# Kernel tuning notes

Hardware: AMD Instinct MI355X
Metric: run time of the kernel (lower is better)

Reference implementation:

```python
import jax, jax.numpy as jnp
import numpy as np

N, E, ET = 50000, 400000, 50000
F, ED, H, L = 64, 32, 128, 2


def _forward(x, edge_attr, target_edge_attr, node_W, node_b, edge_W, edge_b,
             pre_W, pre_b, post_W, post_b, lin_W, lin_b, bn_g, bn_b,
             em1_W, em1_b, em2_W, em2_b, edge_index):
    n = x.shape[0]
    h = node_W.shape[1]
    src, dst = edge_index[0], edge_index[1]
    x = x @ node_W + node_b                      # [N,H]
    ea = edge_attr @ edge_W + edge_b             # [E,H]
    tea = target_edge_attr @ edge_W + edge_b     # [Et,H]

    ones = jnp.ones((src.shape[0],), jnp.float32)
    cnt = jax.ops.segment_sum(ones, dst, num_segments=n)        # in-degree per node
    avg_deg_log = jnp.mean(jnp.log(cnt + 1.0))                  # PyG avg_deg['log'] from deg histogram
    deg = jnp.clip(cnt, 1.0)[:, None]
    amp = jnp.log(deg + 1.0) / avg_deg_log                      # 'amplification' scaler
    att = avg_deg_log / jnp.log(deg + 1.0)                      # 'attenuation' scaler
    cnt_c = jnp.clip(cnt, 1.0)[:, None]
    has = (cnt > 0)[:, None]

    nlayers = pre_W.shape[0]
    for i in range(nlayers):
        # pre-MLP on message cat([x_i(dst), x_j(src), edge_attr]); split matmul avoids [E,3H] concat
        Wd, Ws, We = pre_W[i, :h], pre_W[i, h:2 * h], pre_W[i, 2 * h:]
        m = x[dst] @ Wd + x[src] @ Ws + ea @ We + pre_b[i]      # [E,H]
        s = jax.ops.segment_sum(m, dst, num_segments=n)
        mean = s / cnt_c
        mean2 = jax.ops.segment_sum(m * m, dst, num_segments=n) / cnt_c
        std = jnp.sqrt(jax.nn.relu(mean2 - mean * mean) + 1e-5)  # PyG StdAggregation
        mn = jnp.where(has, jax.ops.segment_min(m, dst, num_segments=n), 0.0)
        mx = jnp.where(has, jax.ops.segment_max(m, dst, num_segments=n), 0.0)
        agg = jnp.concatenate([mean, mn, mx, std], axis=-1)     # [N,4H] aggregator order
        scaled = jnp.concatenate([agg, agg * amp, agg * att], axis=-1)  # [N,12H] scaler order
        # post-MLP on cat([x, scaled]); split matmul
        out = x @ post_W[i, :h] + scaled @ post_W[i, h:] + post_b[i]
        out = out @ lin_W[i] + lin_b[i]
        # BatchNorm (training mode, biased var, eps=1e-5)
        mu = out.mean(axis=0)
        var = jnp.mean((out - mu) ** 2, axis=0)
        bn = bn_g[i] * (out - mu) / jnp.sqrt(var + 1e-5) + bn_b[i]
        x = (x + jax.nn.relu(bn)) / 2
        # edge update: ea + MLP(cat([x[src], x[dst], ea])) / 2
        W1s, W1d, W1e = em1_W[i, :h], em1_W[i, h:2 * h], em1_W[i, 2 * h:]
        hid = jax.nn.relu(x[src] @ W1s + x[dst] @ W1d + ea @ W1e + em1_b[i])
        ea = ea + (hid @ em2_W[i] + em2_b[i]) / 2
    return (x, ea, tea)


def setup_inputs() -> dict:
    key = jax.random.key(0)
    ks = jax.random.split(key, 24)

    def w(k, shape):
        fan_in = shape[-2]
        return (jax.random.normal(k, shape, jnp.float32) / np.sqrt(fan_in)).astype(jnp.float32)

    inp = {
        'x': jax.random.normal(ks[0], (N, F), jnp.float32),
        'edge_attr': jax.random.normal(ks[1], (E, ED), jnp.float32),
        'target_edge_attr': jax.random.normal(ks[2], (ET, ED), jnp.float32),
        'node_W': w(ks[3], (F, H)), 'node_b': jnp.zeros((H,), jnp.float32),
        'edge_W': w(ks[4], (ED, H)), 'edge_b': jnp.zeros((H,), jnp.float32),
        'pre_W': w(ks[5], (L, 3 * H, H)), 'pre_b': jnp.zeros((L, H), jnp.float32),
        'post_W': w(ks[6], (L, 13 * H, H)), 'post_b': jnp.zeros((L, H), jnp.float32),
        'lin_W': w(ks[7], (L, H, H)), 'lin_b': jnp.zeros((L, H), jnp.float32),
        'bn_g': jnp.ones((L, H), jnp.float32), 'bn_b': jnp.zeros((L, H), jnp.float32),
        'em1_W': w(ks[8], (L, 3 * H, H)), 'em1_b': jnp.zeros((L, H), jnp.float32),
        'em2_W': w(ks[9], (L, H, H)), 'em2_b': jnp.zeros((L, H), jnp.float32),
        'edge_index': jax.random.randint(ks[10], (2, E), 0, N, dtype=jnp.int32),
    }
    return inp


def reference(x, edge_attr, target_edge_attr, node_W, node_b, edge_W, edge_b,
              pre_W, pre_b, post_W, post_b, lin_W, lin_b, bn_g, bn_b,
              em1_W, em1_b, em2_W, em2_b, edge_index):
    return _forward(x, edge_attr, target_edge_attr, node_W, node_b, edge_W, edge_b,
                    pre_W, pre_b, post_W, post_b, lin_W, lin_b, bn_g, bn_b,
                    em1_W, em1_b, em2_W, em2_b, edge_index)
```

## Files before the change

kernel.cpp:

```cpp
#include <hip/hip_runtime.h>
#include <math.h>

#define NN  50000
#define NE  400000
#define NTE 50000
#define FIN 64
#define EDIM 32
#define HD  128
#define NL  2
#define SCAN_B ((NN + 255) / 256)

typedef __attribute__((ext_vector_type(8))) short bf16x8;
typedef __attribute__((ext_vector_type(4))) short bf16x4;
typedef __attribute__((ext_vector_type(4))) float f32x4;

static __device__ __forceinline__ unsigned short f2bf(float f) {
    unsigned u = __float_as_uint(f);
    unsigned r = (u + 0x7fffu + ((u >> 16) & 1u)) >> 16;
    return (unsigned short)r;
}
static __device__ __forceinline__ float bfhi2f(unsigned u) { return __uint_as_float(u & 0xffff0000u); }
static __device__ __forceinline__ float bflo2f(unsigned u) { return __uint_as_float(u << 16); }

static __device__ __forceinline__ bf16x8 load_a8(const float* p, bool ok) {
    bf16x8 a = {};
    if (ok) {
        const float4 v0 = *(const float4*)(p);
        const float4 v1 = *(const float4*)(p + 4);
        a[0] = (short)f2bf(v0.x); a[1] = (short)f2bf(v0.y);
        a[2] = (short)f2bf(v0.z); a[3] = (short)f2bf(v0.w);
        a[4] = (short)f2bf(v1.x); a[5] = (short)f2bf(v1.y);
        a[6] = (short)f2bf(v1.z); a[7] = (short)f2bf(v1.w);
    }
    return a;
}
static __device__ __forceinline__ bf16x4 pack4(float4 a) {
    bf16x4 v;
    v[0]=(short)f2bf(a.x); v[1]=(short)f2bf(a.y); v[2]=(short)f2bf(a.z); v[3]=(short)f2bf(a.w);
    return v;
}

__global__ void __launch_bounds__(256) k_packW(const float* __restrict__ W,
        unsigned short* __restrict__ out, int K)
{
    const int tid = blockIdx.x * 256 + threadIdx.x;
    const int total = (K / 32) * 512;
    if (tid >= total) return;
    const int lane = tid & 63, nt = (tid >> 6) & 7, kb = tid >> 9;
    const int k0 = kb * 32 + (lane >> 4) * 8;
    const int col = nt * 16 + (lane & 15);
    bf16x8 v;
    #pragma unroll
    for (int j = 0; j < 8; ++j)
        v[j] = (short)f2bf(W[(size_t)(k0 + j) * HD + col]);
    *(bf16x8*)(out + (size_t)tid * 8) = v;
}

template<int KB>
__global__ void __launch_bounds__(256) k_gemm_T(const float* A,
        const unsigned short* __restrict__ Wpk, const float* __restrict__ bias,
        float* C, int M)
{
    const int t = threadIdx.x, w = t >> 6, l = t & 63;
    const int n = blockIdx.x * 64 + w * 16 + (l & 15);
    const bool ok = n < M;
    const int q = l >> 4;
    const int K = KB * 32;
    f32x4 acc[8] = {};
    #pragma unroll
    for (int kb = 0; kb < KB; ++kb) {
        const bf16x8 b = load_a8(A + (size_t)n * K + kb * 32 + q * 8, ok);
        #pragma unroll
        for (int nt = 0; nt < 8; ++nt) {
            const bf16x8 aW = *(const bf16x8*)(Wpk + (((size_t)(kb * 8 + nt) * 64 + l) << 3));
            acc[nt] = __builtin_amdgcn_mfma_f32_16x16x32_bf16(aW, b, acc[nt], 0, 0, 0);
        }
    }
    if (ok) {
        float* pc = C + (size_t)n * HD + q * 4;
        #pragma unroll
        for (int nt = 0; nt < 8; ++nt) {
            const int col = nt * 16 + q * 4;
            float4 bv = bias ? *(const float4*)(bias + col) : make_float4(0.f,0.f,0.f,0.f);
            float4 o;
            o.x = acc[nt][0] + bv.x; o.y = acc[nt][1] + bv.y;
            o.z = acc[nt][2] + bv.z; o.w = acc[nt][3] + bv.w;
            *(float4*)(pc + nt * 16) = o;
        }
    }
}

template<int KB>
__global__ void __launch_bounds__(256) k_gemm2_T(const float* A,
        const unsigned short* __restrict__ W0, const unsigned short* __restrict__ W1,
        const float* __restrict__ b0, float* C0, float* C1, int M)
{
    const int t = threadIdx.x, w = t >> 6, l = t & 63;
    const int n = blockIdx.x * 64 + w * 16 + (l & 15);
    const bool ok = n < M;
    const int q = l >> 4;
    const int K = KB * 32;
    f32x4 a0[8] = {}, a1[8] = {};
    #pragma unroll
    for (int kb = 0; kb < KB; ++kb) {
        const bf16x8 b = load_a8(A + (size_t)n * K + kb * 32 + q * 8, ok);
        #pragma unroll
        for (int nt = 0; nt < 8; ++nt) {
            const bf16x8 u = *(const bf16x8*)(W0 + (((size_t)(kb * 8 + nt) * 64 + l) << 3));
            const bf16x8 v = *(const bf16x8*)(W1 + (((size_t)(kb * 8 + nt) * 64 + l) << 3));
            a0[nt] = __builtin_amdgcn_mfma_f32_16x16x32_bf16(u, b, a0[nt], 0, 0, 0);
            a1[nt] = __builtin_amdgcn_mfma_f32_16x16x32_bf16(v, b, a1[nt], 0, 0, 0);
        }
    }
    if (ok) {
        float* p0 = C0 + (size_t)n * HD + q * 4;
        float* p1 = C1 + (size_t)n * HD + q * 4;
        #pragma unroll
        for (int nt = 0; nt < 8; ++nt) {
            const int col = nt * 16 + q * 4;
            float4 bv = b0 ? *(const float4*)(b0 + col) : make_float4(0.f,0.f,0.f,0.f);
            float4 o0, o1;
            o0.x = a0[nt][0] + bv.x; o0.y = a0[nt][1] + bv.y;
            o0.z = a0[nt][2] + bv.z; o0.w = a0[nt][3] + bv.w;
            o1.x = a1[nt][0]; o1.y = a1[nt][1]; o1.z = a1[nt][2]; o1.w = a1[nt][3];
            *(float4*)(p0 + nt * 16) = o0;
            *(float4*)(p1 + nt * 16) = o1;
        }
    }
}

__global__ void __launch_bounds__(256) k_count(const int* __restrict__ d, int* __restrict__ cnt, int E)
{
    const int e = blockIdx.x * 256 + threadIdx.x;
    if (e < E) atomicAdd(&cnt[d[e]], 1);
}

__global__ void __launch_bounds__(256) k_avglog(const int* __restrict__ cnt, float* __restrict__ stats)
{
    float s = 0.f;
    for (int n = blockIdx.x * 256 + threadIdx.x; n < NN; n += gridDim.x * 256)
        s += logf((float)cnt[n] + 1.f);
    #pragma unroll
    for (int off = 32; off > 0; off >>= 1) s += __shfl_down(s, off);
    __shared__ float ls[4];
    if ((threadIdx.x & 63) == 0) ls[threadIdx.x >> 6] = s;
    __syncthreads();
    if (threadIdx.x == 0) unsafeAtomicAdd(stats, ls[0] + ls[1] + ls[2] + ls[3]);
}

__global__ void __launch_bounds__(256) k_scan_block(const int* __restrict__ cnt,
        int* __restrict__ incl, int* __restrict__ part)
{
    __shared__ int s[256];
    const int t = threadIdx.x;
    const int i = blockIdx.x * 256 + t;
    const int v = (i < NN) ? cnt[i] : 0;
    s[t] = v;
    __syncthreads();
    #pragma unroll
    for (int off = 1; off < 256; off <<= 1) {
        const int x = (t >= off) ? s[t - off] : 0;
        __syncthreads();
        s[t] += x;
        __syncthreads();
    }
    if (i < NN) incl[i] = s[t];
    if (t == 255) part[blockIdx.x] = s[255];
}

__global__ void __launch_bounds__(256) k_scan_part(const int* __restrict__ part,
        int* __restrict__ poff, int np)
{
    __shared__ int s[256];
    const int t = threadIdx.x;
    const int v = (t < np) ? part[t] : 0;
    s[t] = v;
    __syncthreads();
    #pragma unroll
    for (int off = 1; off < 256; off <<= 1) {
        const int x = (t >= off) ? s[t - off] : 0;
        __syncthreads();
        s[t] += x;
        __syncthreads();
    }
    poff[t] = s[t] - v;
}

__global__ void __launch_bounds__(256) k_scan_add(const int* __restrict__ incl,
        const int* __restrict__ cnt, const int* __restrict__ poff,
        int* __restrict__ row_start, int* __restrict__ cursor)
{
    const int i = blockIdx.x * 256 + threadIdx.x;
    if (i < NN) {
        const int excl = incl[i] - cnt[i] + poff[blockIdx.x];
        row_start[i] = excl;
        cursor[i] = excl;
    }
    if (i == 0) row_start[NN] = NE;
}

__global__ void __launch_bounds__(256) k_scatter(const int* __restrict__ dstp,
        int* cursor, int* __restrict__ sppos)
{
    const int e = blockIdx.x * 256 + threadIdx.x;
    if (e < NE) sppos[e] = atomicAdd(&cursor[dstp[e]], 1);
}

__global__ void __launch_bounds__(256) k_msg_T(const float* __restrict__ ea,
        const unsigned short* __restrict__ Wepk, const float* __restrict__ xs,
        const int* __restrict__ srcp, const int* __restrict__ sppos,
        unsigned short* __restrict__ mbuf)
{
    const int t = threadIdx.x, w = t >> 6, l = t & 63;
    const int e = blockIdx.x * 64 + w * 16 + (l & 15);
    const int q = l >> 4, kq = q * 8;
    f32x4 acc[8] = {};
    #pragma unroll
    for (int kb = 0; kb < 4; ++kb) {
        const bf16x8 bea = load_a8(ea + (size_t)e * HD + kb * 32 + kq, true);
        #pragma unroll
        for (int nt = 0; nt < 8; ++nt) {
            const bf16x8 aW = *(const bf16x8*)(Wepk + (((size_t)(kb * 8 + nt) * 64 + l) << 3));
            acc[nt] = __builtin_amdgcn_mfma_f32_16x16x32_bf16(aW, bea, acc[nt], 0, 0, 0);
        }
    }
    const int sn = srcp[e], sp = sppos[e];
    const float* ps = xs + (size_t)sn * HD + q * 4;
    unsigned short* pm = mbuf + (size_t)sp * HD + q * 4;
    #pragma unroll
    for (int nt = 0; nt < 8; ++nt) {
        const float4 sv = *(const float4*)(ps + nt * 16);
        float4 o;
        o.x = acc[nt][0] + sv.x; o.y = acc[nt][1] + sv.y;
        o.z = acc[nt][2] + sv.z; o.w = acc[nt][3] + sv.w;
        *(bf16x4*)(pm + nt * 16) = pack4(o);
    }
}

__global__ void __launch_bounds__(256) k_agg(const unsigned short* __restrict__ mbuf,
        const int* __restrict__ rs, const float* __restrict__ xd,
        const float* __restrict__ stats, unsigned short* __restrict__ aggb)
{
    const int n = blockIdx.x * 4 + (threadIdx.x >> 6);
    if (n >= NN) return;
    const int lane = threadIdx.x & 63;
    const int c = lane * 2;
    const int s = rs[n], e = rs[n + 1];
    const float2 xv = *(const float2*)(xd + (size_t)n * HD + c);
    float s0=0.f, s1=0.f, q0=0.f, q1=0.f;
    float mn0=INFINITY, mn1=INFINITY, mx0=-INFINITY, mx1=-INFINITY;
    for (int i = s; i < e; ++i) {
        const unsigned u = *(const unsigned*)(mbuf + (size_t)i * HD + c);
        const float v0 = bflo2f(u), v1 = bfhi2f(u);
        s0 += v0; s1 += v1;
        q0 += v0 * v0; q1 += v1 * v1;
        mn0 = fminf(mn0, v0); mn1 = fminf(mn1, v1);
        mx0 = fmaxf(mx0, v0); mx1 = fmaxf(mx1, v1);
    }
    const int deg = e - s;
    const float inv = 1.f / (float)(deg > 1 ? deg : 1);
    const float fd = (float)deg * inv;
    const float m0p = s0 * inv, m1p = s1 * inv;
    const float sd0 = sqrtf(fmaxf(q0 * inv - m0p * m0p, 0.f) + 1e-5f);
    const float sd1 = sqrtf(fmaxf(q1 * inv - m1p * m1p, 0.f) + 1e-5f);
    const bool has = deg > 0;
    const float v0[4] = { m0p + fd * xv.x, has ? mn0 + xv.x : 0.f,
                          has ? mx0 + xv.x : 0.f, sd0 };
    const float v1[4] = { m1p + fd * xv.y, has ? mn1 + xv.y : 0.f,
                          has ? mx1 + xv.y : 0.f, sd1 };
    const float avg = stats[0] * (1.f / (float)NN);
    const float lg = logf(fmaxf((float)deg, 1.f) + 1.f);
    const float amp = lg / avg, att = avg / lg;
    unsigned* a = (unsigned*)(aggb + (size_t)n * 1536 + c);
    #pragma unroll
    for (int sct = 0; sct < 4; ++sct) {
        a[sct * 64]       = (unsigned)f2bf(v0[sct])       | ((unsigned)f2bf(v1[sct]) << 16);
        a[256 + sct * 64] = (unsigned)f2bf(v0[sct] * amp) | ((unsigned)f2bf(v1[sct] * amp) << 16);
        a[512 + sct * 64] = (unsigned)f2bf(v0[sct] * att) | ((unsigned)f2bf(v1[sct] * att) << 16);
    }
}

__global__ void __launch_bounds__(256) k_post_lin_T(const float* __restrict__ x,
        const unsigned short* __restrict__ aggb, const unsigned short* __restrict__ PWpk,
        const float* __restrict__ pb, const unsigned short* __restrict__ LNpk,
        const float* __restrict__ lb, float* __restrict__ outb, int M)
{
    __shared__ unsigned short s_o16[64 * 128];
    const int t = threadIdx.x, w = t >> 6, l = t & 63;
    const int el = w * 16 + (l & 15);
    const int n = blockIdx.x * 64 + el;
    const bool ok = n < M;
    const int q = l >> 4;
    f32x4 acc[8] = {};
    #pragma unroll
    for (int kb = 0; kb < 4; ++kb) {
        const bf16x8 b = load_a8(x + (size_t)n * HD + kb * 32 + q * 8, ok);
        #pragma unroll
        for (int nt = 0; nt < 8; ++nt) {
            const bf16x8 aW = *(const bf16x8*)(PWpk + (((size_t)(kb * 8 + nt) * 64 + l) << 3));
            acc[nt] = __builtin_amdgcn_mfma_f32_16x16x32_bf16(aW, b, acc[nt], 0, 0, 0);
        }
    }
    const unsigned short* arow = aggb + (size_t)n * 1536 + q * 8;
    #pragma unroll 4
    for (int kb = 4; kb < 52; ++kb) {
        bf16x8 b = {};
        if (ok) b = *(const bf16x8*)(arow + (size_t)(kb - 4) * 32);
        #pragma unroll
        for (int nt = 0; nt < 8; ++nt) {
            const bf16x8 aW = *(const bf16x8*)(PWpk + (((size_t)(kb * 8 + nt) * 64 + l) << 3));
            acc[nt] = __builtin_amdgcn_mfma_f32_16x16x32_bf16(aW, b, acc[nt], 0, 0, 0);
        }
    }
    #pragma unroll
    for (int nt = 0; nt < 8; ++nt) {
        const int col = nt * 16 + q * 4;
        const float4 bv = *(const float4*)(pb + col);
        float4 o;
        o.x = acc[nt][0] + bv.x; o.y = acc[nt][1] + bv.y;
        o.z = acc[nt][2] + bv.z; o.w = acc[nt][3] + bv.w;
        const int bcol = nt * 32 + q * 8;
        const int slot = bcol >> 4;
        const int ba = el * 256 + ((slot ^ (el & 7)) << 4) + (bcol & 15);
        *(bf16x4*)((char*)s_o16 + ba) = pack4(o);
    }
    __syncthreads();
    f32x4 acc2[8] = {};
    #pragma unroll
    for (int kb = 0; kb < 4; ++kb) {
        const int slot = kb * 4 + q;
        const int ba = el * 256 + ((slot ^ (el & 7)) << 4);
        const bf16x8 bh = *(const bf16x8*)((const char*)s_o16 + ba);
        #pragma unroll
        for (int nt = 0; nt < 8; ++nt) {
            const bf16x8 aW = *(const bf16x8*)(LNpk + (((size_t)(kb * 8 + nt) * 64 + l) << 3));
            acc2[nt] = __builtin_amdgcn_mfma_f32_16x16x32_bf16(aW, bh, acc2[nt], 0, 0, 0);
        }
    }
    if (ok) {
        float* pc = outb + (size_t)n * HD + q * 4;
        #pragma unroll
        for (int nt = 0; nt < 8; ++nt) {
            const int col = nt * 16 + q * 4;
            const float4 bv = *(const float4*)(lb + col);
            float4 o;
            o.x = acc2[nt][0] + bv.x; o.y = acc2[nt][1] + bv.y;
            o.z = acc2[nt][2] + bv.z; o.w = acc2[nt][3] + bv.w;
            *(float4*)(pc + nt * 16) = o;
        }
    }
}

__global__ void __launch_bounds__(256) k_bnstats(const float* __restrict__ ob,
        float* __restrict__ bs, float* __restrict__ bq, int M)
{
    const int c = threadIdx.x & 127;
    const int gsub = threadIdx.x >> 7;
    float s = 0.f, qq = 0.f;
    for (int rr = blockIdx.x * 2 + gsub; rr < M; rr += gridDim.x * 2) {
        const float v = ob[(size_t)rr * HD + c];
        s += v; qq += v * v;
    }
    __shared__ float ls[2][HD], lq[2][HD];
    ls[gsub][c] = s; lq[gsub][c] = qq;
    __syncthreads();
    if (gsub == 0) {
        unsafeAtomicAdd(&bs[c], ls[0][c] + ls[1][c]);
        unsafeAtomicAdd(&bq[c], lq[0][c] + lq[1][c]);
    }
}

__global__ void __launch_bounds__(256) k_xupdate(float* x, const float* __restrict__ ob,
        const float* __restrict__ bs, const float* __restrict__ bq,
        const float* __restrict__ g, const float* __restrict__ bb)
{
    const int i = blockIdx.x * 256 + threadIdx.x;
    const int c0 = (i & 31) * 4;
    const float4 ov = ((const float4*)ob)[i];
    const float4 xv = ((const float4*)x)[i];
    const float o[4]  = {ov.x, ov.y, ov.z, ov.w};
    const float xo[4] = {xv.x, xv.y, xv.z, xv.w};
    float res[4];
    #pragma unroll
    for (int j = 0; j < 4; ++j) {
        const int c = c0 + j;
        const float mu  = bs[c] * (1.f / (float)NN);
        const float var = bq[c] * (1.f / (float)NN) - mu * mu;
        const float bn  = g[c] * (o[j] - mu) * rsqrtf(var + 1e-5f) + bb[c];
        res[j] = (xo[j] + fmaxf(bn, 0.f)) * 0.5f;
    }
    ((float4*)x)[i] = make_float4(res[0], res[1], res[2], res[3]);
}

__global__ void __launch_bounds__(256) k_edge_upd_T(float* ea,
        const unsigned short* __restrict__ W1epk, const unsigned short* __restrict__ e2pk,
        const float* __restrict__ e2b, const float* __restrict__ xs1,
        const float* __restrict__ xd1, const int* __restrict__ srcp,
        const int* __restrict__ dstp)
{
    __shared__ unsigned short s_hid[64 * 128];
    __shared__ float s_b2[128];
    const int t = threadIdx.x, w = t >> 6, l = t & 63;
    const int row0b = blockIdx.x * 64;
    if (t < 128) s_b2[t] = e2b[t];
    const int el = w * 16 + (l & 15);
    const int e = row0b + el;
    const int q = l >> 4, kq = q * 8;
    f32x4 acc1[8] = {};
    #pragma unroll
    for (int kb = 0; kb < 4; ++kb) {
        const bf16x8 bea = load_a8(ea + (size_t)e * HD + kb * 32 + kq, true);
        #pragma unroll
        for (int nt = 0; nt < 8; ++nt) {
            const bf16x8 aW = *(const bf16x8*)(W1epk + (((size_t)(kb * 8 + nt) * 64 + l) << 3));
            acc1[nt] = __builtin_amdgcn_mfma_f32_16x16x32_bf16(aW, bea, acc1[nt], 0, 0, 0);
        }
    }
    {
        const int sn = srcp[e], dn = dstp[e];
        const float* ps = xs1 + (size_t)sn * HD + q * 4;
        const float* pd = xd1 + (size_t)dn * HD + q * 4;
        #pragma unroll
        for (int nt = 0; nt < 8; ++nt) {
            const float4 sv = *(const float4*)(ps + nt * 16);
            const float4 dv = *(const float4*)(pd + nt * 16);
            float4 h;
            h.x = fmaxf(acc1[nt][0] + sv.x + dv.x, 0.f);
            h.y = fmaxf(acc1[nt][1] + sv.y + dv.y, 0.f);
            h.z = fmaxf(acc1[nt][2] + sv.z + dv.z, 0.f);
            h.w = fmaxf(acc1[nt][3] + sv.w + dv.w, 0.f);
            const int bcol = nt * 32 + q * 8;
            const int slot = bcol >> 4;
            const int ba = el * 256 + ((slot ^ (el & 7)) << 4) + (bcol & 15);
            *(bf16x4*)((char*)s_hid + ba) = pack4(h);
        }
    }
    __syncthreads();
    f32x4 acc2[8] = {};
    #pragma unroll
    for (int kb = 0; kb < 4; ++kb) {
        const int slot = kb * 4 + q;
        const int ba = el * 256 + ((slot ^ (el & 7)) << 4);
        const bf16x8 bh = *(const bf16x8*)((const char*)s_hid + ba);
        #pragma unroll
        for (int nt = 0; nt < 8; ++nt) {
            const bf16x8 aW = *(const bf16x8*)(e2pk + (((size_t)(kb * 8 + nt) * 64 + l) << 3));
            acc2[nt] = __builtin_amdgcn_mfma_f32_16x16x32_bf16(aW, bh, acc2[nt], 0, 0, 0);
        }
    }
    {
        float* pe = ea + (size_t)e * HD + q * 4;
        #pragma unroll
        for (int nt = 0; nt < 8; ++nt) {
            const float4 eo = *(const float4*)(pe + nt * 16);
            const float4 bv = *(const float4*)(&s_b2[nt * 16 + q * 4]);
            float4 o;
            o.x = eo.x + (acc2[nt][0] + bv.x) * 0.5f;
            o.y = eo.y + (acc2[nt][1] + bv.y) * 0.5f;
            o.z = eo.z + (acc2[nt][2] + bv.z) * 0.5f;
            o.w = eo.w + (acc2[nt][3] + bv.w) * 0.5f;
            *(float4*)(pe + nt * 16) = o;
        }
    }
}

extern "C" void kernel_launch(void* const* d_in, const int* in_sizes, int n_in,
                              void* d_out, int out_size, void* d_ws, size_t ws_size,
                              hipStream_t stream)
{
    const float* x0    = (const float*)d_in[0];
    const float* eatr  = (const float*)d_in[1];
    const float* teatr = (const float*)d_in[2];
    const float* nodeW = (const float*)d_in[3];
    const float* nodeb = (const float*)d_in[4];
    const float* edgeW = (const float*)d_in[5];
    const float* edgeb = (const float*)d_in[6];
    const float* preW  = (const float*)d_in[7];
    const float* preb  = (const float*)d_in[8];
    const float* postW = (const float*)d_in[9];
    const float* postb = (const float*)d_in[10];
    const float* linW  = (const float*)d_in[11];
    const float* linb  = (const float*)d_in[12];
    const float* bng   = (const float*)d_in[13];
    const float* bnb   = (const float*)d_in[14];
    const float* em1W  = (const float*)d_in[15];
    const float* em1b  = (const float*)d_in[16];
    const float* em2W  = (const float*)d_in[17];
    const float* em2b  = (const float*)d_in[18];
    const int*   eidx  = (const int*)d_in[19];
    const int* srcp = eidx;
    const int* dstp = eidx + NE;

    float* out_x  = (float*)d_out;
    float* out_ea = out_x + (size_t)NN * HD;
    float* out_te = out_ea + (size_t)NE * HD;

    const size_t NH = (size_t)NN * HD;
    const size_t EH = (size_t)NE * HD;
    float* xd   = (float*)d_ws;
    float* xs   = xd + NH;
    float* outb = xs + NH;
    float* stats = outb + NH;
    int*   cnt      = (int*)(stats + 512);
    int*   row_start = cnt + NN;
    int*   cursor   = row_start + NN + 1;
    int*   tmpincl  = cursor + NN;
    int*   part     = tmpincl + NN;
    int*   poff     = part + 256;
    int*   sppos    = poff + 256;
    unsigned short* mbuf = (unsigned short*)(((uintptr_t)(sppos + NE) + 15) & ~(uintptr_t)15);
    unsigned short* aggb = mbuf + EH;
    unsigned short* pk   = aggb + (size_t)NN * 1536;
    const size_t KBSZ = 512 * 8;
    unsigned short* pkPost = pk;
    unsigned short* pkPre  = pkPost + 104 * KBSZ;
    unsigned short* pkEm1  = pkPre  + 24 * KBSZ;
    unsigned short* pkLin  = pkEm1  + 24 * KBSZ;
    unsigned short* pkEm2  = pkLin  + 8 * KBSZ;
    unsigned short* pkNode = pkEm2  + 8 * KBSZ;
    unsigned short* pkEdge = pkNode + 2 * KBSZ;

    hipMemsetAsync(cnt, 0, NN * sizeof(int), stream);
    hipMemsetAsync(stats, 0, 512 * sizeof(float), stream);

    k_packW<<<208, 256, 0, stream>>>(postW, pkPost, 3328);
    k_packW<<<48, 256, 0, stream>>>(preW,  pkPre,  768);
    k_packW<<<48, 256, 0, stream>>>(em1W,  pkEm1,  768);
    k_packW<<<16, 256, 0, stream>>>(linW,  pkLin,  256);
    k_packW<<<16, 256, 0, stream>>>(em2W,  pkEm2,  256);
    k_packW<<<4, 256, 0, stream>>>(nodeW, pkNode, 64);
    k_packW<<<2, 256, 0, stream>>>(edgeW, pkEdge, 32);

    k_gemm_T<1><<<(NE + 63) / 64, 256, 0, stream>>>(eatr, pkEdge, edgeb, out_ea, NE);
    k_gemm_T<1><<<(NTE + 63) / 64, 256, 0, stream>>>(teatr, pkEdge, edgeb, out_te, NTE);
    k_gemm_T<2><<<(NN + 63) / 64, 256, 0, stream>>>(x0, pkNode, nodeb, out_x, NN);

    k_count<<<(NE + 255) / 256, 256, 0, stream>>>(dstp, cnt, NE);
    k_avglog<<<256, 256, 0, stream>>>(cnt, stats);
    k_scan_block<<<SCAN_B, 256, 0, stream>>>(cnt, tmpincl, part);
    k_scan_part<<<1, 256, 0, stream>>>(part, poff, SCAN_B);
    k_scan_add<<<SCAN_B, 256, 0, stream>>>(tmpincl, cnt, poff, row_start, cursor);
    k_scatter<<<(NE + 255) / 256, 256, 0, stream>>>(dstp, cursor, sppos);

    const int gn = (NN + 63) / 64;
    const int ge = NE / 64;

    for (int l = 0; l < NL; ++l) {
        const unsigned short* Wd_pk  = pkPre + (size_t)(l * 12 + 0) * KBSZ;
        const unsigned short* Ws_pk  = pkPre + (size_t)(l * 12 + 4) * KBSZ;
        const unsigned short* We_pk  = pkPre + (size_t)(l * 12 + 8) * KBSZ;
        const unsigned short* W1s_pk = pkEm1 + (size_t)(l * 12 + 0) * KBSZ;
        const unsigned short* W1d_pk = pkEm1 + (size_t)(l * 12 + 4) * KBSZ;
        const unsigned short* W1e_pk = pkEm1 + (size_t)(l * 12 + 8) * KBSZ;
        const unsigned short* PW_pk  = pkPost + (size_t)l * 52 * KBSZ;
        const unsigned short* lin_pk = pkLin + (size_t)l * 4 * KBSZ;
        const unsigned short* em2_pk = pkEm2 + (size_t)l * 4 * KBSZ;
        const float* pbl = preb + l * HD;
        const float* pob = postb + l * HD;
        const float* lb  = linb + l * HD;
        const float* g_  = bng + l * HD;
        const float* b_  = bnb + l * HD;
        const float* e1b = em1b + l * HD;
        const float* e2b = em2b + l * HD;

        hipMemsetAsync(stats + 128, 0, 256 * sizeof(float), stream);

        k_gemm2_T<4><<<gn, 256, 0, stream>>>(out_x, Wd_pk, Ws_pk, pbl, xd, xs, NN);
        k_msg_T<<<ge, 256, 0, stream>>>(out_ea, We_pk, xs, srcp, sppos, mbuf);
        k_agg<<<(NN + 3) / 4, 256, 0, stream>>>(mbuf, row_start, xd, stats, aggb);
        k_post_lin_T<<<gn, 256, 0, stream>>>(out_x, aggb, PW_pk, pob, lin_pk, lb, outb, NN);
        k_bnstats<<<256, 256, 0, stream>>>(outb, stats + 128, stats + 256, NN);
        k_xupdate<<<NN * 32 / 256, 256, 0, stream>>>(out_x, outb, stats + 128, stats + 256, g_, b_);
        k_gemm2_T<4><<<gn, 256, 0, stream>>>(out_x, W1d_pk, W1s_pk, e1b, xd, xs, NN);
        k_edge_upd_T<<<ge, 256, 0, stream>>>(out_ea, W1e_pk, em2_pk, e2b, xs, xd, srcp, dstp);
    }
}
```

Measured before the change: 1.454 ms.

## Fold edge encoder into layer-0 message weights and store node projections in bf16

For layer 0, the edge-encoder weight and bias are pre-multiplied with the edge part of the pre-MLP weight. The message kernel can then read the raw 32-dim edge attributes instead of the 128-dim encoded ones, which cuts K from 128 to 32 and the per-edge read traffic. Separately, the dst/src node projections xd/xs are written and gathered as bf16 instead of fp32, halving gather bandwidth in the message, aggregation and edge-update kernels. The cost is extra rounding from the bf16 intermediates and from the folded weights being quantised to bf16.

```diff
diff --git a/kernel.cpp b/kernel.cpp
--- a/kernel.cpp
+++ b/kernel.cpp
@@ -56,6 +56,24 @@
     *(bf16x8*)(out + (size_t)tid * 8) = v;
 }
 
+__global__ void __launch_bounds__(256) k_foldW(const float* __restrict__ edgeW,
+        const float* __restrict__ edgeb, const float* __restrict__ We0,
+        float* __restrict__ Wf, float* __restrict__ bf)
+{
+    const int tid = blockIdx.x * 256 + threadIdx.x;
+    if (tid < 4096) {
+        const int k = tid >> 7, c = tid & 127;
+        float s = 0.f;
+        for (int j = 0; j < 128; ++j) s += edgeW[k * HD + j] * We0[(size_t)j * HD + c];
+        Wf[tid] = s;
+    } else if (tid < 4224) {
+        const int c = tid - 4096;
+        float s = 0.f;
+        for (int j = 0; j < 128; ++j) s += edgeb[j] * We0[(size_t)j * HD + c];
+        bf[c] = s;
+    }
+}
+
 template<int KB>
 __global__ void __launch_bounds__(256) k_gemm_T(const float* A,
         const unsigned short* __restrict__ Wpk, const float* __restrict__ bias,
@@ -91,9 +109,9 @@
 }
 
 template<int KB>
-__global__ void __launch_bounds__(256) k_gemm2_T(const float* A,
+__global__ void __launch_bounds__(256) k_gemm2_Tb(const float* A,
         const unsigned short* __restrict__ W0, const unsigned short* __restrict__ W1,
-        const float* __restrict__ b0, float* C0, float* C1, int M)
+        const float* __restrict__ b0, unsigned short* C0, unsigned short* C1, int M)
 {
     const int t = threadIdx.x, w = t >> 6, l = t & 63;
     const int n = blockIdx.x * 64 + w * 16 + (l & 15);
@@ -113,8 +131,8 @@
         }
     }
     if (ok) {
-        float* p0 = C0 + (size_t)n * HD + q * 4;
-        float* p1 = C1 + (size_t)n * HD + q * 4;
+        unsigned short* p0 = C0 + (size_t)n * HD + q * 4;
+        unsigned short* p1 = C1 + (size_t)n * HD + q * 4;
         #pragma unroll
         for (int nt = 0; nt < 8; ++nt) {
             const int col = nt * 16 + q * 4;
@@ -123,8 +141,8 @@
             o0.x = a0[nt][0] + bv.x; o0.y = a0[nt][1] + bv.y;
             o0.z = a0[nt][2] + bv.z; o0.w = a0[nt][3] + bv.w;
             o1.x = a1[nt][0]; o1.y = a1[nt][1]; o1.z = a1[nt][2]; o1.w = a1[nt][3];
-            *(float4*)(p0 + nt * 16) = o0;
-            *(float4*)(p1 + nt * 16) = o1;
+            *(bf16x4*)(p0 + nt * 16) = pack4(o0);
+            *(bf16x4*)(p1 + nt * 16) = pack4(o1);
         }
     }
 }
@@ -206,39 +224,44 @@
     if (e < NE) sppos[e] = atomicAdd(&cursor[dstp[e]], 1);
 }
 
-__global__ void __launch_bounds__(256) k_msg_T(const float* __restrict__ ea,
-        const unsigned short* __restrict__ Wepk, const float* __restrict__ xs,
-        const int* __restrict__ srcp, const int* __restrict__ sppos,
-        unsigned short* __restrict__ mbuf)
+template<int KB>
+__global__ void __launch_bounds__(256) k_msg_T(const float* __restrict__ EA,
+        const unsigned short* __restrict__ Wpk, const float* __restrict__ bias,
+        const unsigned short* __restrict__ xsb, const int* __restrict__ srcp,
+        const int* __restrict__ sppos, unsigned short* __restrict__ mbuf)
 {
     const int t = threadIdx.x, w = t >> 6, l = t & 63;
     const int e = blockIdx.x * 64 + w * 16 + (l & 15);
-    const int q = l >> 4, kq = q * 8;
+    const int q = l >> 4;
     f32x4 acc[8] = {};
     #pragma unroll
-    for (int kb = 0; kb < 4; ++kb) {
-        const bf16x8 bea = load_a8(ea + (size_t)e * HD + kb * 32 + kq, true);
-        #pragma unroll
-        for (int nt = 0; nt < 8; ++nt) {
-            const bf16x8 aW = *(const bf16x8*)(Wepk + (((size_t)(kb * 8 + nt) * 64 + l) << 3));
+    for (int kb = 0; kb < KB; ++kb) {
+        const bf16x8 bea = load_a8(EA + (size_t)e * (KB * 32) + kb * 32 + q * 8, true);
+        #pragma unroll
+        for (int nt = 0; nt < 8; ++nt) {
+            const bf16x8 aW = *(const bf16x8*)(Wpk + (((size_t)(kb * 8 + nt) * 64 + l) << 3));
             acc[nt] = __builtin_amdgcn_mfma_f32_16x16x32_bf16(aW, bea, acc[nt], 0, 0, 0);
         }
     }
     const int sn = srcp[e], sp = sppos[e];
-    const float* ps = xs + (size_t)sn * HD + q * 4;
+    const unsigned short* ps = xsb + (size_t)sn * HD + q * 4;
     unsigned short* pm = mbuf + (size_t)sp * HD + q * 4;
     #pragma unroll
     for (int nt = 0; nt < 8; ++nt) {
-        const float4 sv = *(const float4*)(ps + nt * 16);
+        const uint2 su = *(const uint2*)(ps + nt * 16);
         float4 o;
-        o.x = acc[nt][0] + sv.x; o.y = acc[nt][1] + sv.y;
-        o.z = acc[nt][2] + sv.z; o.w = acc[nt][3] + sv.w;
+        o.x = acc[nt][0] + bflo2f(su.x); o.y = acc[nt][1] + bfhi2f(su.x);
+        o.z = acc[nt][2] + bflo2f(su.y); o.w = acc[nt][3] + bfhi2f(su.y);
+        if (bias) {
+            const float4 bv = *(const float4*)(bias + nt * 16 + q * 4);
+            o.x += bv.x; o.y += bv.y; o.z += bv.z; o.w += bv.w;
+        }
         *(bf16x4*)(pm + nt * 16) = pack4(o);
     }
 }
 
 __global__ void __launch_bounds__(256) k_agg(const unsigned short* __restrict__ mbuf,
-        const int* __restrict__ rs, const float* __restrict__ xd,
+        const int* __restrict__ rs, const unsigned short* __restrict__ xdb,
         const float* __restrict__ stats, unsigned short* __restrict__ aggb)
 {
     const int n = blockIdx.x * 4 + (threadIdx.x >> 6);
@@ -246,7 +269,8 @@
     const int lane = threadIdx.x & 63;
     const int c = lane * 2;
     const int s = rs[n], e = rs[n + 1];
-    const float2 xv = *(const float2*)(xd + (size_t)n * HD + c);
+    const unsigned xu = *(const unsigned*)(xdb + (size_t)n * HD + c);
+    const float xv0 = bflo2f(xu), xv1 = bfhi2f(xu);
     float s0=0.f, s1=0.f, q0=0.f, q1=0.f;
     float mn0=INFINITY, mn1=INFINITY, mx0=-INFINITY, mx1=-INFINITY;
     for (int i = s; i < e; ++i) {
@@ -264,10 +288,10 @@
     const float sd0 = sqrtf(fmaxf(q0 * inv - m0p * m0p, 0.f) + 1e-5f);
     const float sd1 = sqrtf(fmaxf(q1 * inv - m1p * m1p, 0.f) + 1e-5f);
     const bool has = deg > 0;
-    const float v0[4] = { m0p + fd * xv.x, has ? mn0 + xv.x : 0.f,
-                          has ? mx0 + xv.x : 0.f, sd0 };
-    const float v1[4] = { m1p + fd * xv.y, has ? mn1 + xv.y : 0.f,
-                          has ? mx1 + xv.y : 0.f, sd1 };
+    const float v0[4] = { m0p + fd * xv0, has ? mn0 + xv0 : 0.f,
+                          has ? mx0 + xv0 : 0.f, sd0 };
+    const float v1[4] = { m1p + fd * xv1, has ? mn1 + xv1 : 0.f,
+                          has ? mx1 + xv1 : 0.f, sd1 };
     const float avg = stats[0] * (1.f / (float)NN);
     const float lg = logf(fmaxf((float)deg, 1.f) + 1.f);
     const float amp = lg / avg, att = avg / lg;
@@ -394,8 +418,8 @@
 
 __global__ void __launch_bounds__(256) k_edge_upd_T(float* ea,
         const unsigned short* __restrict__ W1epk, const unsigned short* __restrict__ e2pk,
-        const float* __restrict__ e2b, const float* __restrict__ xs1,
-        const float* __restrict__ xd1, const int* __restrict__ srcp,
+        const float* __restrict__ e2b, const unsigned short* __restrict__ xs1b,
+        const unsigned short* __restrict__ xd1b, const int* __restrict__ srcp,
         const int* __restrict__ dstp)
 {
     __shared__ unsigned short s_hid[64 * 128];
@@ -418,17 +442,17 @@
     }
     {
         const int sn = srcp[e], dn = dstp[e];
-        const float* ps = xs1 + (size_t)sn * HD + q * 4;
-        const float* pd = xd1 + (size_t)dn * HD + q * 4;
-        #pragma unroll
-        for (int nt = 0; nt < 8; ++nt) {
-            const float4 sv = *(const float4*)(ps + nt * 16);
-            const float4 dv = *(const float4*)(pd + nt * 16);
+        const unsigned short* ps = xs1b + (size_t)sn * HD + q * 4;
+        const unsigned short* pd = xd1b + (size_t)dn * HD + q * 4;
+        #pragma unroll
+        for (int nt = 0; nt < 8; ++nt) {
+            const uint2 su = *(const uint2*)(ps + nt * 16);
+            const uint2 du = *(const uint2*)(pd + nt * 16);
             float4 h;
-            h.x = fmaxf(acc1[nt][0] + sv.x + dv.x, 0.f);
-            h.y = fmaxf(acc1[nt][1] + sv.y + dv.y, 0.f);
-            h.z = fmaxf(acc1[nt][2] + sv.z + dv.z, 0.f);
-            h.w = fmaxf(acc1[nt][3] + sv.w + dv.w, 0.f);
+            h.x = fmaxf(acc1[nt][0] + bflo2f(su.x) + bflo2f(du.x), 0.f);
+            h.y = fmaxf(acc1[nt][1] + bfhi2f(su.x) + bfhi2f(du.x), 0.f);
+            h.z = fmaxf(acc1[nt][2] + bflo2f(su.y) + bflo2f(du.y), 0.f);
+            h.w = fmaxf(acc1[nt][3] + bfhi2f(su.y) + bfhi2f(du.y), 0.f);
             const int bcol = nt * 32 + q * 8;
             const int slot = bcol >> 4;
             const int ba = el * 256 + ((slot ^ (el & 7)) << 4) + (bcol & 15);
@@ -497,11 +521,13 @@
 
     const size_t NH = (size_t)NN * HD;
     const size_t EH = (size_t)NE * HD;
-    float* xd   = (float*)d_ws;
-    float* xs   = xd + NH;
-    float* outb = xs + NH;
+    unsigned short* xdb = (unsigned short*)d_ws;
+    unsigned short* xsb = xdb + NH;
+    float* outb  = (float*)(xsb + NH);
     float* stats = outb + NH;
-    int*   cnt      = (int*)(stats + 512);
+    float* Wf    = stats + 512;
+    float* bfold = Wf + 4096;
+    int*   cnt      = (int*)(bfold + 128);
     int*   row_start = cnt + NN;
     int*   cursor   = row_start + NN + 1;
     int*   tmpincl  = cursor + NN;
@@ -519,6 +545,7 @@
     unsigned short* pkEm2  = pkLin  + 8 * KBSZ;
     unsigned short* pkNode = pkEm2  + 8 * KBSZ;
     unsigned short* pkEdge = pkNode + 2 * KBSZ;
+    unsigned short* pkWe0f = pkEdge + 1 * KBSZ;
 
     hipMemsetAsync(cnt, 0, NN * sizeof(int), stream);
     hipMemsetAsync(stats, 0, 512 * sizeof(float), stream);
@@ -530,6 +557,8 @@
     k_packW<<<16, 256, 0, stream>>>(em2W,  pkEm2,  256);
     k_packW<<<4, 256, 0, stream>>>(nodeW, pkNode, 64);
     k_packW<<<2, 256, 0, stream>>>(edgeW, pkEdge, 32);
+    k_foldW<<<17, 256, 0, stream>>>(edgeW, edgeb, preW + 256 * HD, Wf, bfold);
+    k_packW<<<2, 256, 0, stream>>>(Wf, pkWe0f, 32);
 
     k_gemm_T<1><<<(NE + 63) / 64, 256, 0, stream>>>(eatr, pkEdge, edgeb, out_ea, NE);
     k_gemm_T<1><<<(NTE + 63) / 64, 256, 0, stream>>>(teatr, pkEdge, edgeb, out_te, NTE);
@@ -565,13 +594,16 @@
 
         hipMemsetAsync(stats + 128, 0, 256 * sizeof(float), stream);
 
-        k_gemm2_T<4><<<gn, 256, 0, stream>>>(out_x, Wd_pk, Ws_pk, pbl, xd, xs, NN);
-        k_msg_T<<<ge, 256, 0, stream>>>(out_ea, We_pk, xs, srcp, sppos, mbuf);
-        k_agg<<<(NN + 3) / 4, 256, 0, stream>>>(mbuf, row_start, xd, stats, aggb);
+        k_gemm2_Tb<4><<<gn, 256, 0, stream>>>(out_x, Wd_pk, Ws_pk, pbl, xdb, xsb, NN);
+        if (l == 0)
+            k_msg_T<1><<<ge, 256, 0, stream>>>(eatr, pkWe0f, bfold, xsb, srcp, sppos, mbuf);
+        else
+            k_msg_T<4><<<ge, 256, 0, stream>>>(out_ea, We_pk, nullptr, xsb, srcp, sppos, mbuf);
+        k_agg<<<(NN + 3) / 4, 256, 0, stream>>>(mbuf, row_start, xdb, stats, aggb);
         k_post_lin_T<<<gn, 256, 0, stream>>>(out_x, aggb, PW_pk, pob, lin_pk, lb, outb, NN);
         k_bnstats<<<256, 256, 0, stream>>>(outb, stats + 128, stats + 256, NN);
         k_xupdate<<<NN * 32 / 256, 256, 0, stream>>>(out_x, outb, stats + 128, stats + 256, g_, b_);
-        k_gemm2_T<4><<<gn, 256, 0, stream>>>(out_x, W1d_pk, W1s_pk, e1b, xd, xs, NN);
-        k_edge_upd_T<<<ge, 256, 0, stream>>>(out_ea, W1e_pk, em2_pk, e2b, xs, xd, srcp, dstp);
-    }
-}
+        k_gemm2_Tb<4><<<gn, 256, 0, stream>>>(out_x, W1d_pk, W1s_pk, e1b, xdb, xsb, NN);
+        k_edge_upd_T<<<ge, 256, 0, stream>>>(out_ea, W1e_pk, em2_pk, e2b, xsb, xdb, srcp, dstp);
+    }
+}
```

Result: faster. 1.404 ms (-3.4%).
